# Optimization experiments

Measured on AMD Instinct MI355X. Metric: run time of the kernel, lower is better.

## Reference

```python
import jax, jax.numpy as jnp
import numpy as np

N_NODES = 50000
N_EDGES = 800000
IN_DIM = 128
ADD = 8
HIDDEN = 256
OUT_DIM = 128


def gcn_conv(x, src, dst, W, b, n_nodes):
    """PyG GCNConv: linear -> sym-normalized scatter-add with self-loops -> bias."""
    loop = jnp.arange(n_nodes, dtype=src.dtype)
    s = jnp.concatenate([src, loop])
    d = jnp.concatenate([dst, loop])
    deg = jax.ops.segment_sum(jnp.ones(s.shape[0], dtype=x.dtype), d, num_segments=n_nodes)
    dinv = jnp.where(deg > 0, jax.lax.rsqrt(deg), 0.0)
    norm = dinv[s] * dinv[d]                       # [E+N]
    h = x @ W                                      # [N, F_out]
    msg = h[s] * norm[:, None]                     # [E+N, F_out]
    out = jax.ops.segment_sum(msg, d, num_segments=n_nodes)
    return out + b


def prelu(x, a):
    return jnp.where(x >= 0, x, a * x)


def setup_inputs() -> dict:
    key = jax.random.key(0)
    ks = jax.random.split(key, 8)
    x = jax.random.normal(ks[0], (N_NODES, IN_DIM), dtype=jnp.float32)
    edge_index = jax.random.randint(ks[1], (2, N_EDGES), 0, N_NODES, dtype=jnp.int64)
    id_vec = jax.random.normal(ks[2], (ADD,), dtype=jnp.float32)
    # Glorot-ish init for linear weights, PReLU slope 0.25 (torch default)
    W1 = jax.random.normal(ks[3], (IN_DIM + ADD, HIDDEN), dtype=jnp.float32) * 0.05
    b1 = jnp.zeros((HIDDEN,), dtype=jnp.float32)
    a1 = jnp.full((HIDDEN,), 0.25, dtype=jnp.float32)
    W2 = jax.random.normal(ks[4], (HIDDEN, OUT_DIM), dtype=jnp.float32) * 0.05
    b2 = jnp.zeros((OUT_DIM,), dtype=jnp.float32)
    a2 = jnp.full((OUT_DIM,), 0.25, dtype=jnp.float32)
    return {"x": x, "edge_index": edge_index, "id": id_vec,
            "W1": W1, "b1": b1, "a1": a1, "W2": W2, "b2": b2, "a2": a2}


def reference(x, edge_index, id, W1, b1, a1, W2, b2, a2):
    n = x.shape[0]
    src, dst = edge_index[0], edge_index[1]
    # tile id vector onto every node and concat along features
    xi = jnp.concatenate([x, jnp.broadcast_to(id[None, :], (n, id.shape[0]))], axis=1)
    h = gcn_conv(xi, src, dst, W1, b1, n)
    h = prelu(h, a1)
    h = gcn_conv(h, src, dst, W2, b2, n)
    h = prelu(h, a2)
    return h
```

## Files before the change

kernel.cpp:

```cpp
#include <hip/hip_runtime.h>


constexpr int NN = 50000;
constexpr int NE = 800000;
constexpr int NBUCK = 196;
constexpr int TILE = 2048;
constexpr int NSCAT = (NE + TILE - 1) / TILE;

typedef __attribute__((ext_vector_type(8))) short short8;
typedef __attribute__((ext_vector_type(4))) float floatx4;

__device__ inline void bsplit(float v, unsigned short& hi, unsigned short& lo) {
  unsigned u = __float_as_uint(v);
  hi = (unsigned short)(u >> 16);
  float rem = v - __uint_as_float(u & 0xffff0000u);
  lo = (unsigned short)(__float_as_uint(rem) >> 16);
}

__device__ inline unsigned short bf16_rtne(float v) {
  unsigned u = __float_as_uint(v);
  return (unsigned short)((u + 0x7fffu + ((u >> 16) & 1u)) >> 16);
}

__device__ inline float bflo(unsigned u) { return __uint_as_float(u << 16); }
__device__ inline float bfhi(unsigned u) { return __uint_as_float(u & 0xffff0000u); }


__global__ __launch_bounds__(256) void tile_count_kernel(const int* __restrict__ ei,
                                                         int* __restrict__ tilecnt) {
  __shared__ int h[NBUCK];
  int t = threadIdx.x;
  for (int i = t; i < NBUCK; i += 256) h[i] = 0;
  __syncthreads();
  int base = blockIdx.x * TILE;
  int end = base + TILE; if (end > NE) end = NE;
  for (int e = base + t; e < end; e += 256) atomicAdd(&h[ei[NE + e] >> 8], 1);
  __syncthreads();
  for (int i = t; i < NBUCK; i += 256) tilecnt[blockIdx.x * NBUCK + i] = h[i];
}

__global__ __launch_bounds__(256) void tile_scan_a_kernel(const int* __restrict__ tilecnt,
                                                          int* __restrict__ tpre,
                                                          int* __restrict__ bcnt) {
  __shared__ int sm[256];
  int b = blockIdx.x, t = threadIdx.x;
  int i0 = 2 * t, i1 = 2 * t + 1;
  int v0 = (i0 < NSCAT) ? tilecnt[i0 * NBUCK + b] : 0;
  int v1 = (i1 < NSCAT) ? tilecnt[i1 * NBUCK + b] : 0;
  int s = v0 + v1;
  sm[t] = s;
  __syncthreads();
  for (int off = 1; off < 256; off <<= 1) {
    int u = (t >= off) ? sm[t - off] : 0;
    __syncthreads();
    sm[t] += u;
    __syncthreads();
  }
  int ex = sm[t] - s;
  if (i0 < NSCAT) tpre[i0 * NBUCK + b] = ex;
  if (i1 < NSCAT) tpre[i1 * NBUCK + b] = ex + v0;
  if (t == 255) bcnt[b] = sm[255];
}

__global__ void bucket_base_kernel(const int* __restrict__ bcnt, int* __restrict__ bbase) {
  __shared__ int sm[256];
  int t = threadIdx.x;
  int v = (t < NBUCK) ? bcnt[t] : 0;
  sm[t] = v;
  __syncthreads();
  for (int off = 1; off < 256; off <<= 1) {
    int u = (t >= off) ? sm[t - off] : 0;
    __syncthreads();
    sm[t] += u;
    __syncthreads();
  }
  if (t < NBUCK) bbase[t] = sm[t] - v;
}

__global__ __launch_bounds__(256) void bucket_scatter_kernel(
    const int* __restrict__ ei, const int* __restrict__ tilecnt,
    const int* __restrict__ tpre, const int* __restrict__ bbase,
    unsigned* __restrict__ ebuf) {
  __shared__ int lbase[NBUCK], gb[NBUCK], lcur[NBUCK], ssc[256];
  __shared__ unsigned stage[TILE];
  int t = threadIdx.x;
  int tile = blockIdx.x;
  int base = tile * TILE;
  int cntTile = NE - base; if (cntTile > TILE) cntTile = TILE;
  int h = (t < NBUCK) ? tilecnt[tile * NBUCK + t] : 0;
  ssc[t] = h;
  __syncthreads();
  for (int off = 1; off < 256; off <<= 1) {
    int u = (t >= off) ? ssc[t - off] : 0;
    __syncthreads();
    ssc[t] += u;
    __syncthreads();
  }
  if (t < NBUCK) {
    int ex = ssc[t] - h;
    lbase[t] = ex;
    lcur[t] = ex;
    gb[t] = bbase[t] + tpre[tile * NBUCK + t];
  }
  __syncthreads();
  for (int e = base + t; e < base + cntTile; e += 256) {
    int s = ei[e];
    int d = ei[NE + e];
    int b = d >> 8;
    int pos = atomicAdd(&lcur[b], 1);
    stage[pos] = ((unsigned)(d & 255) << 16) | (unsigned)s;
  }
  __syncthreads();
  for (int i = t; i < cntTile; i += 256) {
    int lo = 0, hi = NBUCK - 1;
    while (lo < hi) {
      int mid = (lo + hi + 1) >> 1;
      if (lbase[mid] <= i) lo = mid; else hi = mid - 1;
    }
    ebuf[gb[lo] + (i - lbase[lo])] = stage[i];
  }
}

__global__ __launch_bounds__(256) void bucket_csr_kernel(
    const unsigned* __restrict__ ebuf, const int* __restrict__ bbase,
    const int* __restrict__ bcnt, int* __restrict__ offs, int* __restrict__ col,
    float* __restrict__ dinv) {
  __shared__ int cnt[256], cur[256], sums[256];
  int b = blockIdx.x, t = threadIdx.x;
  int node0 = b << 8;
  cnt[t] = 0;
  __syncthreads();
  int g0 = bbase[b], g1 = g0 + bcnt[b];
  for (int i = g0 + t; i < g1; i += 256) atomicAdd(&cnt[ebuf[i] >> 16], 1);
  __syncthreads();
  int c = cnt[t];
  sums[t] = c;
  __syncthreads();
  for (int off = 1; off < 256; off <<= 1) {
    int u = (t >= off) ? sums[t - off] : 0;
    __syncthreads();
    sums[t] += u;
    __syncthreads();
  }
  int ex = sums[t] - c;
  cur[t] = ex;
  int node = node0 + t;
  if (node < NN) {
    offs[node] = g0 + ex;
    dinv[node] = rsqrtf((float)(c + 1));
  }
  __syncthreads();
  for (int i = g0 + t; i < g1; i += 256) {
    unsigned v = ebuf[i];
    int pos = atomicAdd(&cur[v >> 16], 1);
    col[g0 + pos] = (int)(v & 0xffffu);
  }
  if (b == 0 && t == 0) offs[NN] = NE;
}

__global__ __launch_bounds__(256) void post_csr_kernel(
    const float* __restrict__ x, const float* __restrict__ dinv,
    const int* __restrict__ offs, const int* __restrict__ col,
    unsigned short* __restrict__ xsb, float* __restrict__ Svec) {
  int id = blockIdx.x * 256 + threadIdx.x;
  if (id < NN * 32) {
    float dd = dinv[id >> 5];
    float4 v = ((const float4*)x)[id];
    ushort4 o;
    o.x = bf16_rtne(v.x * dd);
    o.y = bf16_rtne(v.y * dd);
    o.z = bf16_rtne(v.z * dd);
    o.w = bf16_rtne(v.w * dd);
    ((ushort4*)xsb)[id] = o;
  } else {
    int d = id - NN * 32;
    if (d < NN) {
      float s = 0.f;
      int end = offs[d + 1];
      for (int p = offs[d]; p < end; ++p) s += dinv[col[p]];
      float dd = dinv[d];
      Svec[d] = dd * (dd + s);
    }
  }
}

template <int K, int N>
__device__ inline void pack_one(const float* __restrict__ W, unsigned short* __restrict__ Bhi,
                                unsigned short* __restrict__ Blo, int id) {
  constexpr int KC = K / 32;
  int j = id & 7;
  int lane = (id >> 3) & 63;
  int rest = id >> 9;
  int c = rest % KC;
  int nt = rest / KC;
  int k = c * 32 + (lane >> 4) * 8 + j;
  int n = nt * 16 + (lane & 15);
  unsigned short hi, lo;
  bsplit(W[(size_t)k * N + n], hi, lo);
  Bhi[id] = hi;
  Blo[id] = lo;
}

__global__ void prep_weights_kernel(const float* __restrict__ W1, const float* __restrict__ W2,
                                    const float* __restrict__ idv,
                                    unsigned short* __restrict__ B1hi, unsigned short* __restrict__ B1lo,
                                    unsigned short* __restrict__ B2hi, unsigned short* __restrict__ B2lo,
                                    float* __restrict__ cvec) {
  int id = blockIdx.x * 256 + threadIdx.x;
  if (id < 32768) {
    pack_one<128, 256>(W1, B1hi, B1lo, id);
  } else if (id < 65536) {
    pack_one<256, 128>(W2, B2hi, B2lo, id - 32768);
  } else if (id < 65536 + 256) {
    int m = id - 65536;
    float c = 0.f;
#pragma unroll
    for (int j = 0; j < 8; ++j) c += idv[j] * W1[(128 + j) * 256 + m];
    cvec[m] = c;
  }
}

template <int MODE>
__global__ __launch_bounds__(256) void agg_kernel(
    const unsigned short* __restrict__ in, const float* __restrict__ dinv,
    const int* __restrict__ offs, const int* __restrict__ col,
    const float* __restrict__ bias, const float* __restrict__ alpha,
    unsigned short* __restrict__ outhi, unsigned short* __restrict__ outlo,
    float* __restrict__ outf) {
  const uint2* inb = (const uint2*)in;
  int t = threadIdx.x;
  int node = blockIdx.x * 4 + (t >> 6);
  int lane = t & 63;
  int r = lane & 31;
  int half = lane >> 5;
  int beg = offs[node], end = offs[node + 1];

  float4 a0 = make_float4(0.f, 0.f, 0.f, 0.f);
  float4 a1 = make_float4(0.f, 0.f, 0.f, 0.f);
  float4 a2 = make_float4(0.f, 0.f, 0.f, 0.f);
  float4 a3 = make_float4(0.f, 0.f, 0.f, 0.f);
  int p = beg + half;
  for (; p + 14 < end; p += 16) {
    int s0 = col[p];      int s1 = col[p + 2];
    int s2 = col[p + 4];  int s3 = col[p + 6];
    int s4 = col[p + 8];  int s5 = col[p + 10];
    int s6 = col[p + 12]; int s7 = col[p + 14];
    uint2 v0 = inb[(size_t)s0 * 32 + r];
    uint2 v1 = inb[(size_t)s1 * 32 + r];
    uint2 v2 = inb[(size_t)s2 * 32 + r];
    uint2 v3 = inb[(size_t)s3 * 32 + r];
    uint2 v4 = inb[(size_t)s4 * 32 + r];
    uint2 v5 = inb[(size_t)s5 * 32 + r];
    uint2 v6 = inb[(size_t)s6 * 32 + r];
    uint2 v7 = inb[(size_t)s7 * 32 + r];
    a0.x += bflo(v0.x); a0.y += bfhi(v0.x); a0.z += bflo(v0.y); a0.w += bfhi(v0.y);
    a1.x += bflo(v1.x); a1.y += bfhi(v1.x); a1.z += bflo(v1.y); a1.w += bfhi(v1.y);
    a2.x += bflo(v2.x); a2.y += bfhi(v2.x); a2.z += bflo(v2.y); a2.w += bfhi(v2.y);
    a3.x += bflo(v3.x); a3.y += bfhi(v3.x); a3.z += bflo(v3.y); a3.w += bfhi(v3.y);
    a0.x += bflo(v4.x); a0.y += bfhi(v4.x); a0.z += bflo(v4.y); a0.w += bfhi(v4.y);
    a1.x += bflo(v5.x); a1.y += bfhi(v5.x); a1.z += bflo(v5.y); a1.w += bfhi(v5.y);
    a2.x += bflo(v6.x); a2.y += bfhi(v6.x); a2.z += bflo(v6.y); a2.w += bfhi(v6.y);
    a3.x += bflo(v7.x); a3.y += bfhi(v7.x); a3.z += bflo(v7.y); a3.w += bfhi(v7.y);
  }
  for (; p + 2 < end; p += 4) {
    int s0 = col[p];
    int s1 = col[p + 2];
    uint2 v0 = inb[(size_t)s0 * 32 + r];
    uint2 v1 = inb[(size_t)s1 * 32 + r];
    a0.x += bflo(v0.x); a0.y += bfhi(v0.x); a0.z += bflo(v0.y); a0.w += bfhi(v0.y);
    a1.x += bflo(v1.x); a1.y += bfhi(v1.x); a1.z += bflo(v1.y); a1.w += bfhi(v1.y);
  }
  if (p < end) {
    uint2 v0 = inb[(size_t)col[p] * 32 + r];
    a0.x += bflo(v0.x); a0.y += bfhi(v0.x); a0.z += bflo(v0.y); a0.w += bfhi(v0.y);
  }
  float4 acc = make_float4((a0.x + a1.x) + (a2.x + a3.x), (a0.y + a1.y) + (a2.y + a3.y),
                           (a0.z + a1.z) + (a2.z + a3.z), (a0.w + a1.w) + (a2.w + a3.w));
  acc.x += __shfl_xor(acc.x, 32);
  acc.y += __shfl_xor(acc.y, 32);
  acc.z += __shfl_xor(acc.z, 32);
  acc.w += __shfl_xor(acc.w, 32);

  float dd = dinv[node];
  if (half == 0) {
    uint2 sv = inb[(size_t)node * 32 + r];
    acc.x = dd * (acc.x + bflo(sv.x));
    acc.y = dd * (acc.y + bfhi(sv.x));
    acc.z = dd * (acc.z + bflo(sv.y));
    acc.w = dd * (acc.w + bfhi(sv.y));
    if (MODE == 0) {
      ushort4 h4, l4;
      bsplit(acc.x, h4.x, l4.x);
      bsplit(acc.y, h4.y, l4.y);
      bsplit(acc.z, h4.z, l4.z);
      bsplit(acc.w, h4.w, l4.w);
      ((ushort4*)outhi)[(size_t)node * 32 + r] = h4;
      ((ushort4*)outlo)[(size_t)node * 32 + r] = l4;
    } else {
      float4 b = ((const float4*)bias)[r];
      float4 al = ((const float4*)alpha)[r];
      acc.x += b.x; acc.y += b.y; acc.z += b.z; acc.w += b.w;
      acc.x = (acc.x >= 0.f) ? acc.x : al.x * acc.x;
      acc.y = (acc.y >= 0.f) ? acc.y : al.y * acc.y;
      acc.z = (acc.z >= 0.f) ? acc.z : al.z * acc.z;
      acc.w = (acc.w >= 0.f) ? acc.w : al.w * acc.w;
      ((float4*)outf)[(size_t)node * 32 + r] = acc;
    }
  }
}

template <int K, int N, int MODE>
__global__ __launch_bounds__(256) void gemm_mfma_kernel(
    const unsigned short* __restrict__ Ahi, const unsigned short* __restrict__ Alo,
    const unsigned short* __restrict__ Bhi, const unsigned short* __restrict__ Blo,
    const float* __restrict__ Svec, const float* __restrict__ cvec,
    const float* __restrict__ bias, const float* __restrict__ alpha,
    const float* __restrict__ rowscale,
    unsigned short* __restrict__ Chi, unsigned short* __restrict__ Clo,
    unsigned short* __restrict__ Cb) {
  constexpr int KC = K / 32;
  constexpr int NT = N / 16;
  int wave = threadIdx.x >> 6;
  int lane = threadIdx.x & 63;
  int row0 = blockIdx.x * 64 + wave * 16;
  if (row0 >= NN) return;
  int m = lane & 15, quad = lane >> 4;
  int arow = row0 + m;

  short8 ah[KC], al[KC];
  const unsigned short* ap = Ahi + (size_t)arow * K + quad * 8;
  const unsigned short* alp = Alo + (size_t)arow * K + quad * 8;
#pragma unroll
  for (int c = 0; c < KC; ++c) {
    ah[c] = *(const short8*)(ap + c * 32);
    al[c] = *(const short8*)(alp + c * 32);
  }

  float sv[4];
#pragma unroll
  for (int i = 0; i < 4; ++i) {
    int r = row0 + quad * 4 + i;
    sv[i] = (MODE == 1) ? Svec[r] : rowscale[r];
  }

#pragma unroll 1
  for (int nt = 0; nt < NT; ++nt) {
    floatx4 acc = {0.f, 0.f, 0.f, 0.f};
#pragma unroll
    for (int c = 0; c < KC; ++c) {
      short8 bh = *(const short8*)(Bhi + ((size_t)(nt * KC + c) * 64 + lane) * 8);
      short8 bl = *(const short8*)(Blo + ((size_t)(nt * KC + c) * 64 + lane) * 8);
      acc = __builtin_amdgcn_mfma_f32_16x16x32_bf16(ah[c], bh, acc, 0, 0, 0);
      acc = __builtin_amdgcn_mfma_f32_16x16x32_bf16(ah[c], bl, acc, 0, 0, 0);
      acc = __builtin_amdgcn_mfma_f32_16x16x32_bf16(al[c], bh, acc, 0, 0, 0);
    }
    int c0 = nt * 16 + m;
    if (MODE == 1) {
      float cv = cvec[c0], bb = bias[c0], aa = alpha[c0];
#pragma unroll
      for (int i = 0; i < 4; ++i) {
        int r = row0 + quad * 4 + i;
        float v = acc[i] + sv[i] * cv + bb;
        v = (v >= 0.f) ? v : aa * v;
        unsigned short hi, lo;
        bsplit(v, hi, lo);
        Chi[(size_t)r * N + c0] = hi;
        Clo[(size_t)r * N + c0] = lo;
      }
    } else {
#pragma unroll
      for (int i = 0; i < 4; ++i) {
        int r = row0 + quad * 4 + i;
        Cb[(size_t)r * N + c0] = bf16_rtne(acc[i] * sv[i]);
      }
    }
  }
}

extern "C" void kernel_launch(void* const* d_in, const int* in_sizes, int n_in,
                              void* d_out, int out_size, void* d_ws, size_t ws_size,
                              hipStream_t stream) {
  const float* x = (const float*)d_in[0];
  const int* ei = (const int*)d_in[1];
  const float* idv = (const float*)d_in[2];
  const float* W1 = (const float*)d_in[3];
  const float* b1 = (const float*)d_in[4];
  const float* a1 = (const float*)d_in[5];
  const float* W2 = (const float*)d_in[6];
  const float* b2 = (const float*)d_in[7];
  const float* a2 = (const float*)d_in[8];
  float* out = (float*)d_out;

  char* w = (char*)d_ws;
  size_t off = 0;
  auto alloc = [&](size_t bytes) -> void* {
    void* p = w + off;
    off += bytes;
    off = (off + 255) & ~(size_t)255;
    return p;
  };
  int* tilecnt = (int*)alloc((size_t)NSCAT * NBUCK * 4);
  int* tpre = (int*)alloc((size_t)NSCAT * NBUCK * 4);
  int* bbase = (int*)alloc((size_t)NBUCK * 4);
  int* bcnt = (int*)alloc((size_t)NBUCK * 4);
  unsigned* ebuf = (unsigned*)alloc((size_t)NE * 4);
  float* dinv = (float*)alloc((size_t)NN * 4);
  float* Svec = (float*)alloc((size_t)NN * 4);
  int* offs = (int*)alloc((size_t)(NN + 1) * 4);
  int* col = (int*)alloc((size_t)NE * 4);
  float* cvec = (float*)alloc(256 * 4);
  unsigned short* xsb = (unsigned short*)alloc((size_t)NN * 128 * 2);
  unsigned short* aggxhi = (unsigned short*)alloc((size_t)NN * 128 * 2);
  unsigned short* aggxlo = (unsigned short*)alloc((size_t)NN * 128 * 2);
  unsigned short* h1hi = (unsigned short*)alloc((size_t)NN * 256 * 2);
  unsigned short* h1lo = (unsigned short*)alloc((size_t)NN * 256 * 2);
  unsigned short* h2b = (unsigned short*)alloc((size_t)NN * 128 * 2);
  unsigned short* B1hi = (unsigned short*)alloc(128 * 256 * 2);
  unsigned short* B1lo = (unsigned short*)alloc(128 * 256 * 2);
  unsigned short* B2hi = (unsigned short*)alloc(256 * 128 * 2);
  unsigned short* B2lo = (unsigned short*)alloc(256 * 128 * 2);

  tile_count_kernel<<<NSCAT, 256, 0, stream>>>(ei, tilecnt);
  tile_scan_a_kernel<<<NBUCK, 256, 0, stream>>>(tilecnt, tpre, bcnt);
  bucket_base_kernel<<<1, 256, 0, stream>>>(bcnt, bbase);
  bucket_scatter_kernel<<<NSCAT, 256, 0, stream>>>(ei, tilecnt, tpre, bbase, ebuf);
  bucket_csr_kernel<<<NBUCK, 256, 0, stream>>>(ebuf, bbase, bcnt, offs, col, dinv);

  prep_weights_kernel<<<(65536 + 256 + 255) / 256, 256, 0, stream>>>(
      W1, W2, idv, B1hi, B1lo, B2hi, B2lo, cvec);
  post_csr_kernel<<<(NN * 32 + NN + 255) / 256, 256, 0, stream>>>(
      x, dinv, offs, col, xsb, Svec);

  agg_kernel<0><<<NN / 4, 256, 0, stream>>>(xsb, dinv, offs, col, nullptr, nullptr,
                                            aggxhi, aggxlo, nullptr);

  gemm_mfma_kernel<128, 256, 1><<<(NN + 63) / 64, 256, 0, stream>>>(
      aggxhi, aggxlo, B1hi, B1lo, Svec, cvec, b1, a1, nullptr, h1hi, h1lo, nullptr);

  gemm_mfma_kernel<256, 128, 2><<<(NN + 63) / 64, 256, 0, stream>>>(
      h1hi, h1lo, B2hi, B2lo, nullptr, nullptr, nullptr, nullptr, dinv,
      nullptr, nullptr, h2b);

  agg_kernel<1><<<NN / 4, 256, 0, stream>>>(h2b, dinv, offs, col, b2, a2,
                                            nullptr, nullptr, out);
}
```

Measured before the change: 273.4 us.

## Fuse the two dense GEMMs, keeping the hidden layer in LDS

Merges the first GEMM (with bias, PReLU and hi/lo split) and the second GEMM into one kernel. Each wave writes its 16x256 hidden tile into swizzled shared memory and reloads it as A operands for the second GEMM. This avoids writing and re-reading the 50000x256 hi/lo intermediate in global memory and removes one launch. The cost is 64KB of LDS per block, which limits occupancy, and a longer serial kernel per wave.

```diff
diff --git a/kernel.cpp b/kernel.cpp
--- a/kernel.cpp
+++ b/kernel.cpp
@@ -309,70 +309,89 @@
   }
 }
 
-template <int K, int N, int MODE>
-__global__ __launch_bounds__(256) void gemm_mfma_kernel(
+__global__ __launch_bounds__(256) void gemm_fused_kernel(
     const unsigned short* __restrict__ Ahi, const unsigned short* __restrict__ Alo,
-    const unsigned short* __restrict__ Bhi, const unsigned short* __restrict__ Blo,
+    const unsigned short* __restrict__ B1hi, const unsigned short* __restrict__ B1lo,
+    const unsigned short* __restrict__ B2hi, const unsigned short* __restrict__ B2lo,
     const float* __restrict__ Svec, const float* __restrict__ cvec,
     const float* __restrict__ bias, const float* __restrict__ alpha,
-    const float* __restrict__ rowscale,
-    unsigned short* __restrict__ Chi, unsigned short* __restrict__ Clo,
-    unsigned short* __restrict__ Cb) {
-  constexpr int KC = K / 32;
-  constexpr int NT = N / 16;
+    const float* __restrict__ dinv, unsigned short* __restrict__ h2b) {
+  constexpr int K1 = 128, KC1 = 4, NT1 = 16;
+  constexpr int KC2 = 8, NT2 = 8;
+  __shared__ __attribute__((aligned(16))) char smem[4 * 16384];
+
   int wave = threadIdx.x >> 6;
   int lane = threadIdx.x & 63;
   int row0 = blockIdx.x * 64 + wave * 16;
   if (row0 >= NN) return;
   int m = lane & 15, quad = lane >> 4;
-  int arow = row0 + m;
-
-  short8 ah[KC], al[KC];
-  const unsigned short* ap = Ahi + (size_t)arow * K + quad * 8;
-  const unsigned short* alp = Alo + (size_t)arow * K + quad * 8;
-#pragma unroll
-  for (int c = 0; c < KC; ++c) {
+  char* wb = smem + wave * 16384;
+
+  short8 ah[KC1], al[KC1];
+  const unsigned short* ap = Ahi + (size_t)(row0 + m) * K1 + quad * 8;
+  const unsigned short* alp = Alo + (size_t)(row0 + m) * K1 + quad * 8;
+#pragma unroll
+  for (int c = 0; c < KC1; ++c) {
     ah[c] = *(const short8*)(ap + c * 32);
     al[c] = *(const short8*)(alp + c * 32);
   }
-
   float sv[4];
 #pragma unroll
-  for (int i = 0; i < 4; ++i) {
-    int r = row0 + quad * 4 + i;
-    sv[i] = (MODE == 1) ? Svec[r] : rowscale[r];
-  }
+  for (int i = 0; i < 4; ++i) sv[i] = Svec[row0 + quad * 4 + i];
 
 #pragma unroll 1
-  for (int nt = 0; nt < NT; ++nt) {
+  for (int nt = 0; nt < NT1; ++nt) {
     floatx4 acc = {0.f, 0.f, 0.f, 0.f};
 #pragma unroll
-    for (int c = 0; c < KC; ++c) {
-      short8 bh = *(const short8*)(Bhi + ((size_t)(nt * KC + c) * 64 + lane) * 8);
-      short8 bl = *(const short8*)(Blo + ((size_t)(nt * KC + c) * 64 + lane) * 8);
+    for (int c = 0; c < KC1; ++c) {
+      short8 bh = *(const short8*)(B1hi + ((size_t)(nt * KC1 + c) * 64 + lane) * 8);
+      short8 bl = *(const short8*)(B1lo + ((size_t)(nt * KC1 + c) * 64 + lane) * 8);
       acc = __builtin_amdgcn_mfma_f32_16x16x32_bf16(ah[c], bh, acc, 0, 0, 0);
       acc = __builtin_amdgcn_mfma_f32_16x16x32_bf16(ah[c], bl, acc, 0, 0, 0);
       acc = __builtin_amdgcn_mfma_f32_16x16x32_bf16(al[c], bh, acc, 0, 0, 0);
     }
     int c0 = nt * 16 + m;
-    if (MODE == 1) {
-      float cv = cvec[c0], bb = bias[c0], aa = alpha[c0];
-#pragma unroll
-      for (int i = 0; i < 4; ++i) {
-        int r = row0 + quad * 4 + i;
-        float v = acc[i] + sv[i] * cv + bb;
-        v = (v >= 0.f) ? v : aa * v;
-        unsigned short hi, lo;
-        bsplit(v, hi, lo);
-        Chi[(size_t)r * N + c0] = hi;
-        Clo[(size_t)r * N + c0] = lo;
-      }
-    } else {
-#pragma unroll
-      for (int i = 0; i < 4; ++i) {
-        int r = row0 + quad * 4 + i;
-        Cb[(size_t)r * N + c0] = bf16_rtne(acc[i] * sv[i]);
-      }
+    float cv = cvec[c0], bb = bias[c0], aa = alpha[c0];
+#pragma unroll
+    for (int i = 0; i < 4; ++i) {
+      float v = acc[i] + sv[i] * cv + bb;
+      v = (v >= 0.f) ? v : aa * v;
+      unsigned short hi, lo;
+      bsplit(v, hi, lo);
+      int row16 = quad * 4 + i;
+      int off = row16 * 512 + ((c0 * 2) ^ ((row16 & 7) << 4));
+      *(unsigned short*)(wb + off) = hi;
+      *(unsigned short*)(wb + 8192 + off) = lo;
+    }
+  }
+
+  short8 ah2[KC2], al2[KC2];
+#pragma unroll
+  for (int c = 0; c < KC2; ++c) {
+    int off = m * 512 + ((c * 64 + quad * 16) ^ ((m & 7) << 4));
+    ah2[c] = *(const short8*)(wb + off);
+    al2[c] = *(const short8*)(wb + 8192 + off);
+  }
+  float dv[4];
+#pragma unroll
+  for (int i = 0; i < 4; ++i) dv[i] = dinv[row0 + quad * 4 + i];
+
+#pragma unroll 1
+  for (int nt = 0; nt < NT2; ++nt) {
+    floatx4 acc = {0.f, 0.f, 0.f, 0.f};
+#pragma unroll
+    for (int c = 0; c < KC2; ++c) {
+      short8 bh = *(const short8*)(B2hi + ((size_t)(nt * KC2 + c) * 64 + lane) * 8);
+      short8 bl = *(const short8*)(B2lo + ((size_t)(nt * KC2 + c) * 64 + lane) * 8);
+      acc = __builtin_amdgcn_mfma_f32_16x16x32_bf16(ah2[c], bh, acc, 0, 0, 0);
+      acc = __builtin_amdgcn_mfma_f32_16x16x32_bf16(ah2[c], bl, acc, 0, 0, 0);
+      acc = __builtin_amdgcn_mfma_f32_16x16x32_bf16(al2[c], bh, acc, 0, 0, 0);
+    }
+    int c0 = nt * 16 + m;
+#pragma unroll
+    for (int i = 0; i < 4; ++i) {
+      int r = row0 + quad * 4 + i;
+      h2b[(size_t)r * 128 + c0] = bf16_rtne(acc[i] * dv[i]);
     }
   }
 }
@@ -412,8 +431,6 @@
   unsigned short* xsb = (unsigned short*)alloc((size_t)NN * 128 * 2);
   unsigned short* aggxhi = (unsigned short*)alloc((size_t)NN * 128 * 2);
   unsigned short* aggxlo = (unsigned short*)alloc((size_t)NN * 128 * 2);
-  unsigned short* h1hi = (unsigned short*)alloc((size_t)NN * 256 * 2);
-  unsigned short* h1lo = (unsigned short*)alloc((size_t)NN * 256 * 2);
   unsigned short* h2b = (unsigned short*)alloc((size_t)NN * 128 * 2);
   unsigned short* B1hi = (unsigned short*)alloc(128 * 256 * 2);
   unsigned short* B1lo = (unsigned short*)alloc(128 * 256 * 2);
@@ -434,12 +451,8 @@
   agg_kernel<0><<<NN / 4, 256, 0, stream>>>(xsb, dinv, offs, col, nullptr, nullptr,
                                             aggxhi, aggxlo, nullptr);
 
-  gemm_mfma_kernel<128, 256, 1><<<(NN + 63) / 64, 256, 0, stream>>>(
-      aggxhi, aggxlo, B1hi, B1lo, Svec, cvec, b1, a1, nullptr, h1hi, h1lo, nullptr);
-
-  gemm_mfma_kernel<256, 128, 2><<<(NN + 63) / 64, 256, 0, stream>>>(
-      h1hi, h1lo, B2hi, B2lo, nullptr, nullptr, nullptr, nullptr, dinv,
-      nullptr, nullptr, h2b);
+  gemm_fused_kernel<<<(NN + 63) / 64, 256, 0, stream>>>(
+      aggxhi, aggxlo, B1hi, B1lo, B2hi, B2lo, Svec, cvec, b1, a1, dinv, h2b);
 
   agg_kernel<1><<<NN / 4, 256, 0, stream>>>(h2b, dinv, offs, col, b2, a2,
                                             nullptr, nullptr, out);
```

Result: faster. 256.4 us (-6.2%).
